# Kernel tuning notes

Hardware: AMD Instinct MI355X
Metric: run time of the kernel (lower is better)

Reference implementation:

```python
import jax, jax.numpy as jnp
import numpy as np

DIMS = [64, 32, 12, 8, 6, 2]


def setup_inputs() -> dict:
    key = jax.random.key(0)
    ks = jax.random.split(key, 1 + 2 * (len(DIMS) - 1))
    inp = {"x": jax.random.normal(ks[0], (1048576, DIMS[0]), dtype=jnp.float32)}
    for i in range(len(DIMS) - 1):
        fan_in = DIMS[i]
        bound = 1.0 / np.sqrt(fan_in)
        inp[f"W{i}"] = jax.random.uniform(ks[1 + 2 * i], (DIMS[i], DIMS[i + 1]), jnp.float32, -bound, bound)
        inp[f"b{i}"] = jax.random.uniform(ks[2 + 2 * i], (DIMS[i + 1],), jnp.float32, -bound, bound)
    return inp


def reference(x, W0, b0, W1, b1, W2, b2, W3, b3, W4, b4):
    # 5-layer Linear+ReLU chain (final layer has no ReLU), matching nn.Sequential.
    h = jax.nn.relu(x @ W0 + b0)
    h = jax.nn.relu(h @ W1 + b1)
    h = jax.nn.relu(h @ W2 + b2)
    h = jax.nn.relu(h @ W3 + b3)
    return h @ W4 + b4  # [B, 2]
```

## Files before the change

### kernel.cpp

```cpp
#include <hip/hip_runtime.h>


typedef __attribute__((ext_vector_type(8))) short short8;
typedef __attribute__((ext_vector_type(16))) float f32x16;
typedef __attribute__((ext_vector_type(4))) unsigned uint4v;
typedef __attribute__((address_space(3))) void* as3p;
typedef const __attribute__((address_space(1))) void* as1p;

#define BLOCK 64
#define NT 4

__device__ __forceinline__ unsigned fbits(float x) {
    return __builtin_bit_cast(unsigned, x);
}
__device__ __forceinline__ float asf(unsigned u) {
    return __builtin_bit_cast(float, u);
}
__device__ __forceinline__ unsigned packhi(unsigned ua, unsigned ub) {
    return __builtin_amdgcn_perm(ub, ua, 0x07060302u);
}
__device__ __forceinline__ short8 mk_hi(const float* f) {
    uint4v w;
#pragma unroll
    for (int t = 0; t < 4; ++t)
        w[t] = packhi(fbits(f[2 * t]), fbits(f[2 * t + 1]));
    return __builtin_bit_cast(short8, w);
}
__device__ __forceinline__ short8 mk_lo(const float* f) {
    uint4v w;
#pragma unroll
    for (int t = 0; t < 4; ++t) {
        const float la = f[2 * t]     - asf(fbits(f[2 * t])     & 0xFFFF0000u);
        const float lb = f[2 * t + 1] - asf(fbits(f[2 * t + 1]) & 0xFFFF0000u);
        w[t] = packhi(fbits(la), fbits(lb));
    }
    return __builtin_bit_cast(short8, w);
}
#define MFMA(A, B, C) __builtin_amdgcn_mfma_f32_32x32x16_bf16(A, B, C, 0, 0, 0)

template <int IN, int OUT, bool RELU>
__device__ __forceinline__ void layer(const float* __restrict__ W,
                                      const float* __restrict__ b,
                                      const float* h_in, float* h_out) {
#pragma unroll
    for (int o = 0; o < OUT; ++o) h_out[o] = b[o];
#pragma unroll
    for (int i = 0; i < IN; ++i) {
        const float v = h_in[i];
#pragma unroll
        for (int o = 0; o < OUT; ++o)
            h_out[o] = fmaf(v, W[i * OUT + o], h_out[o]);
    }
    if (RELU) {
#pragma unroll
        for (int o = 0; o < OUT; ++o) h_out[o] = fmaxf(h_out[o], 0.0f);
    }
}

__global__ __launch_bounds__(BLOCK, 2) void mlp_kernel(
        const float* __restrict__ x,
        const float* __restrict__ W0, const float* __restrict__ b0,
        const float* __restrict__ W1, const float* __restrict__ b1,
        const float* __restrict__ W2, const float* __restrict__ b2,
        const float* __restrict__ W3, const float* __restrict__ b3,
        const float* __restrict__ W4, const float* __restrict__ b4,
        float* __restrict__ out, int nrows) {
    extern __shared__ char lds[];
    char* buf0 = lds;
    char* buf1 = lds + 8192;

    const int lane = threadIdx.x;
    const long long row0 = (long long)blockIdx.x * (NT * 64);
    const char* xbase = reinterpret_cast<const char*>(x + row0 * 64);

    const int hh = lane >> 3;
    const int qq = (lane & 7) ^ hh;
    const int stage_off = (2 * hh + (qq >> 2)) * 256 + (qq & 3) * 16;

    const int r0 = lane & 31;
    const int hA = lane >> 5;
    auto lds_off = [](int r, int u) {
        const int R = r >> 1, p = r & 1;
        return R * 128 + (((u + 4 * p) ^ (R & 7)) << 4);
    };
    const int aoff0 = lds_off(r0, 2 * hA);
    const int aoff1 = lds_off(r0, 2 * hA + 1);
    const int aoff2 = lds_off(r0 + 32, 2 * hA);
    const int aoff3 = lds_off(r0 + 32, 2 * hA + 1);

    const int colB = lane & 31;
    short8 W0h_, W0l_, W1h_, W1l_, W2h_, W2l_, W3h_, W3l_;
    {
        float wf[8];
#define LOADB(s, BH, BL)                                                \
        {                                                               \
            _Pragma("unroll")                                           \
            for (int j = 0; j < 8; ++j)                                 \
                wf[j] = W0[((s) * 16 + 8 * hA + j) * 32 + colB];        \
            BH = mk_hi(wf);                                             \
            BL = mk_lo(wf);                                             \
        }
        LOADB(0, W0h_, W0l_)
        LOADB(1, W1h_, W1l_)
        LOADB(2, W2h_, W2l_)
        LOADB(3, W3h_, W3l_)
#undef LOADB
    }

    auto STAGE8 = [&](int gc, char* buf) {
        const char* s0 = xbase + (gc >> 1) * (64 * 256) + (gc & 1) * 128 +
                         stage_off;
#pragma unroll
        for (int k = 0; k < 4; ++k)
            __builtin_amdgcn_global_load_lds((as1p)(s0 + k * 4096),
                                             (as3p)(buf + k * 1024), 16, 0, 0);
#pragma unroll
        for (int k = 0; k < 4; ++k)
            __builtin_amdgcn_global_load_lds((as1p)(s0 + 64 + k * 4096),
                                             (as3p)(buf + 4096 + k * 1024),
                                             16, 0, 0);
    };

    STAGE8(0, buf0);

#pragma unroll 1
    for (int tt = 0; tt < NT; ++tt) {
        f32x16 accA, accB;
#pragma unroll
        for (int r = 0; r < 16; ++r) { accA[r] = 0.0f; accB[r] = 0.0f; }

#define KSTEP(CUR, SUB, WH, WL)                                            \
        {                                                                  \
            float fA[8], fB[8];                                            \
            const float4 q0 = *reinterpret_cast<const float4*>(CUR + SUB + aoff0); \
            const float4 q1 = *reinterpret_cast<const float4*>(CUR + SUB + aoff1); \
            const float4 q2 = *reinterpret_cast<const float4*>(CUR + SUB + aoff2); \
            const float4 q3 = *reinterpret_cast<const float4*>(CUR + SUB + aoff3); \
            fA[0]=q0.x; fA[1]=q0.y; fA[2]=q0.z; fA[3]=q0.w;                \
            fA[4]=q1.x; fA[5]=q1.y; fA[6]=q1.z; fA[7]=q1.w;                \
            fB[0]=q2.x; fB[1]=q2.y; fB[2]=q2.z; fB[3]=q2.w;                \
            fB[4]=q3.x; fB[5]=q3.y; fB[6]=q3.z; fB[7]=q3.w;                \
            const short8 Xh = mk_hi(fA), Xl = mk_lo(fA);                   \
            const short8 Yh = mk_hi(fB), Yl = mk_lo(fB);                   \
            accA = MFMA(WH, Xh, accA);                                     \
            accA = MFMA(WL, Xh, accA);                                     \
            accA = MFMA(WH, Xl, accA);                                     \
            accB = MFMA(WH, Yh, accB);                                     \
            accB = MFMA(WL, Yh, accB);                                     \
            accB = MFMA(WH, Yl, accB);                                     \
        }
#define PHASE(c, WH0, WL0, WH1, WL1)                                       \
        {                                                                  \
            const int gc = tt * 2 + (c);                                   \
            char* cur = ((c) & 1) ? buf1 : buf0;                           \
            char* oth = ((c) & 1) ? buf0 : buf1;                           \
            if (gc + 1 < NT * 2) {                                         \
                STAGE8(gc + 1, oth);                                       \
                asm volatile("s_waitcnt vmcnt(8)" ::: "memory");           \
            } else {                                                       \
                asm volatile("s_waitcnt vmcnt(0)" ::: "memory");           \
            }                                                              \
            __builtin_amdgcn_sched_barrier(0);                             \
            KSTEP(cur, 0,    WH0, WL0)                                     \
            KSTEP(cur, 4096, WH1, WL1)                                     \
        }

        PHASE(0, W0h_, W0l_, W1h_, W1l_)
        PHASE(1, W2h_, W2l_, W3h_, W3l_)
#undef PHASE
#undef KSTEP

        float xr[32];
#pragma unroll
        for (int reg = 0; reg < 16; ++reg) {
            float a = accA[reg];
            float b = accB[reg];
            asm("v_permlane32_swap_b32 %0, %1" : "+v"(a), "+v"(b));
            const int f0 = (reg & 3) + 8 * (reg >> 2);
            xr[f0]     = fmaxf(a + b0[f0],     0.0f);
            xr[f0 + 4] = fmaxf(b + b0[f0 + 4], 0.0f);
        }

        float h1[12], h2[8], h3[6], h4[2];
        layer<32, 12, true>(W1, b1, xr, h1);
        layer<12, 8, true>(W2, b2, h1, h2);
        layer<8, 6, true>(W3, b3, h2, h3);
        layer<6, 2, false>(W4, b4, h3, h4);

        reinterpret_cast<float2*>(out)[row0 + tt * 64 + lane] =
            make_float2(h4[0], h4[1]);
    }
}

extern "C" void kernel_launch(void* const* d_in, const int* in_sizes, int n_in,
                              void* d_out, int out_size, void* d_ws, size_t ws_size,
                              hipStream_t stream) {
    const float* x  = (const float*)d_in[0];
    const float* W0 = (const float*)d_in[1];
    const float* b0 = (const float*)d_in[2];
    const float* W1 = (const float*)d_in[3];
    const float* b1 = (const float*)d_in[4];
    const float* W2 = (const float*)d_in[5];
    const float* b2 = (const float*)d_in[6];
    const float* W3 = (const float*)d_in[7];
    const float* b3 = (const float*)d_in[8];
    const float* W4 = (const float*)d_in[9];
    const float* b4 = (const float*)d_in[10];
    float* out = (float*)d_out;

    const int nrows = in_sizes[0] / 64;
    const int rows_per_block = NT * 64;
    const int grid = nrows / rows_per_block;
    const size_t shmem = 16384;

    mlp_kernel<<<grid, BLOCK, shmem, stream>>>(x, W0, b0, W1, b1, W2, b2,
                                               W3, b3, W4, b4, out, nrows);
}
```

Baseline: 66.25 us.

## Stage contiguous row blocks into padded LDS and raise waves per SIMD

Each staging step now copies 32 full contiguous rows (8 KB) from global memory into LDS. A 48-byte pad every four rows replaces the XOR swizzle on column halves. The two accumulators now come from two row-half stages, each running all four K-steps, instead of two column-chunk phases. The launch bound is raised to allow three blocks per SIMD. The aims are more sequential global loads, simpler LDS addressing and more latency hiding, at the cost of a slightly larger LDS footprint and tighter register limits.

```diff
diff --git a/kernel.cpp b/kernel.cpp
--- a/kernel.cpp
+++ b/kernel.cpp
@@ -9,6 +9,7 @@
 
 #define BLOCK 64
 #define NT 4
+#define BUFSZ 8576
 
 __device__ __forceinline__ unsigned fbits(float x) {
     return __builtin_bit_cast(unsigned, x);
@@ -57,7 +58,7 @@
     }
 }
 
-__global__ __launch_bounds__(BLOCK, 2) void mlp_kernel(
+__global__ __launch_bounds__(BLOCK, 3) void mlp_kernel(
         const float* __restrict__ x,
         const float* __restrict__ W0, const float* __restrict__ b0,
         const float* __restrict__ W1, const float* __restrict__ b1,
@@ -66,27 +67,16 @@
         const float* __restrict__ W4, const float* __restrict__ b4,
         float* __restrict__ out, int nrows) {
     extern __shared__ char lds[];
-    char* buf0 = lds;
-    char* buf1 = lds + 8192;
+    char* const bA = lds;
+    char* const bB = lds + BUFSZ;
 
     const int lane = threadIdx.x;
     const long long row0 = (long long)blockIdx.x * (NT * 64);
     const char* xbase = reinterpret_cast<const char*>(x + row0 * 64);
 
-    const int hh = lane >> 3;
-    const int qq = (lane & 7) ^ hh;
-    const int stage_off = (2 * hh + (qq >> 2)) * 256 + (qq & 3) * 16;
-
     const int r0 = lane & 31;
     const int hA = lane >> 5;
-    auto lds_off = [](int r, int u) {
-        const int R = r >> 1, p = r & 1;
-        return R * 128 + (((u + 4 * p) ^ (R & 7)) << 4);
-    };
-    const int aoff0 = lds_off(r0, 2 * hA);
-    const int aoff1 = lds_off(r0, 2 * hA + 1);
-    const int aoff2 = lds_off(r0 + 32, 2 * hA);
-    const int aoff3 = lds_off(r0 + 32, 2 * hA + 1);
+    const int rb = r0 * 256 + (r0 >> 2) * 48 + hA * 32;
 
     const int colB = lane & 31;
     short8 W0h_, W0l_, W1h_, W1l_, W2h_, W2l_, W3h_, W3l_;
@@ -107,21 +97,15 @@
 #undef LOADB
     }
 
-    auto STAGE8 = [&](int gc, char* buf) {
-        const char* s0 = xbase + (gc >> 1) * (64 * 256) + (gc & 1) * 128 +
-                         stage_off;
-#pragma unroll
-        for (int k = 0; k < 4; ++k)
-            __builtin_amdgcn_global_load_lds((as1p)(s0 + k * 4096),
-                                             (as3p)(buf + k * 1024), 16, 0, 0);
-#pragma unroll
-        for (int k = 0; k < 4; ++k)
-            __builtin_amdgcn_global_load_lds((as1p)(s0 + 64 + k * 4096),
-                                             (as3p)(buf + 4096 + k * 1024),
-                                             16, 0, 0);
+    auto STAGEH = [&](int g, char* buf) {
+        const char* s0 = xbase + g * 8192 + lane * 16;
+#pragma unroll
+        for (int k = 0; k < 8; ++k)
+            __builtin_amdgcn_global_load_lds((as1p)(s0 + k * 1024),
+                                             (as3p)(buf + k * 1072), 16, 0, 0);
     };
 
-    STAGE8(0, buf0);
+    STAGEH(0, bA);
 
 #pragma unroll 1
     for (int tt = 0; tt < NT; ++tt) {
@@ -129,45 +113,43 @@
 #pragma unroll
         for (int r = 0; r < 16; ++r) { accA[r] = 0.0f; accB[r] = 0.0f; }
 
-#define KSTEP(CUR, SUB, WH, WL)                                            \
+#define KSTEP(CUR, s, WH, WL, ACC)                                         \
         {                                                                  \
-            float fA[8], fB[8];                                            \
-            const float4 q0 = *reinterpret_cast<const float4*>(CUR + SUB + aoff0); \
-            const float4 q1 = *reinterpret_cast<const float4*>(CUR + SUB + aoff1); \
-            const float4 q2 = *reinterpret_cast<const float4*>(CUR + SUB + aoff2); \
-            const float4 q3 = *reinterpret_cast<const float4*>(CUR + SUB + aoff3); \
-            fA[0]=q0.x; fA[1]=q0.y; fA[2]=q0.z; fA[3]=q0.w;                \
-            fA[4]=q1.x; fA[5]=q1.y; fA[6]=q1.z; fA[7]=q1.w;                \
-            fB[0]=q2.x; fB[1]=q2.y; fB[2]=q2.z; fB[3]=q2.w;                \
-            fB[4]=q3.x; fB[5]=q3.y; fB[6]=q3.z; fB[7]=q3.w;                \
-            const short8 Xh = mk_hi(fA), Xl = mk_lo(fA);                   \
-            const short8 Yh = mk_hi(fB), Yl = mk_lo(fB);                   \
-            accA = MFMA(WH, Xh, accA);                                     \
-            accA = MFMA(WL, Xh, accA);                                     \
-            accA = MFMA(WH, Xl, accA);                                     \
-            accB = MFMA(WH, Yh, accB);                                     \
-            accB = MFMA(WL, Yh, accB);                                     \
-            accB = MFMA(WH, Yl, accB);                                     \
-        }
-#define PHASE(c, WH0, WL0, WH1, WL1)                                       \
-        {                                                                  \
-            const int gc = tt * 2 + (c);                                   \
-            char* cur = ((c) & 1) ? buf1 : buf0;                           \
-            char* oth = ((c) & 1) ? buf0 : buf1;                           \
-            if (gc + 1 < NT * 2) {                                         \
-                STAGE8(gc + 1, oth);                                       \
-                asm volatile("s_waitcnt vmcnt(8)" ::: "memory");           \
-            } else {                                                       \
-                asm volatile("s_waitcnt vmcnt(0)" ::: "memory");           \
-            }                                                              \
-            __builtin_amdgcn_sched_barrier(0);                             \
-            KSTEP(cur, 0,    WH0, WL0)                                     \
-            KSTEP(cur, 4096, WH1, WL1)                                     \
-        }
-
-        PHASE(0, W0h_, W0l_, W1h_, W1l_)
-        PHASE(1, W2h_, W2l_, W3h_, W3l_)
-#undef PHASE
+            float f[8];                                                    \
+            const float4 q0 = *reinterpret_cast<const float4*>(            \
+                (CUR) + rb + (s) * 64);                                    \
+            const float4 q1 = *reinterpret_cast<const float4*>(            \
+                (CUR) + rb + (s) * 64 + 16);                               \
+            f[0]=q0.x; f[1]=q0.y; f[2]=q0.z; f[3]=q0.w;                    \
+            f[4]=q1.x; f[5]=q1.y; f[6]=q1.z; f[7]=q1.w;                    \
+            const short8 Xh = mk_hi(f), Xl = mk_lo(f);                     \
+            ACC = MFMA(WH, Xh, ACC);                                       \
+            ACC = MFMA(WL, Xh, ACC);                                       \
+            ACC = MFMA(WH, Xl, ACC);                                       \
+        }
+
+        {
+            STAGEH(2 * tt + 1, bB);
+            asm volatile("s_waitcnt vmcnt(8)" ::: "memory");
+            __builtin_amdgcn_sched_barrier(0);
+            KSTEP(bA, 0, W0h_, W0l_, accA)
+            KSTEP(bA, 1, W1h_, W1l_, accA)
+            KSTEP(bA, 2, W2h_, W2l_, accA)
+            KSTEP(bA, 3, W3h_, W3l_, accA)
+        }
+        {
+            if (tt + 1 < NT) {
+                STAGEH(2 * tt + 2, bA);
+                asm volatile("s_waitcnt vmcnt(8)" ::: "memory");
+            } else {
+                asm volatile("s_waitcnt vmcnt(0)" ::: "memory");
+            }
+            __builtin_amdgcn_sched_barrier(0);
+            KSTEP(bB, 0, W0h_, W0l_, accB)
+            KSTEP(bB, 1, W1h_, W1l_, accB)
+            KSTEP(bB, 2, W2h_, W2l_, accB)
+            KSTEP(bB, 3, W3h_, W3l_, accB)
+        }
 #undef KSTEP
 
         float xr[32];
@@ -211,7 +193,7 @@
     const int nrows = in_sizes[0] / 64;
     const int rows_per_block = NT * 64;
     const int grid = nrows / rows_per_block;
-    const size_t shmem = 16384;
+    const size_t shmem = 2 * BUFSZ;
 
     mlp_kernel<<<grid, BLOCK, shmem, stream>>>(x, W0, b0, W1, b1, W2, b2,
                                                W3, b3, W4, b4, out, nrows);
```

New measurement: 66.47 us. No clear change (+0.3%).
